# Performance work log

Measured on AMD Instinct MI355X. Metric: run time of the kernel, lower is better.

The kernel has to match this reference:

```python
import jax, jax.numpy as jnp
import numpy as np
import math

B, C, H, W = 8, 64, 256, 256
E, NH = 256, 8
HD = E // NH  # 32


def get_coords(h, w):
    xx, yy = jnp.meshgrid(jnp.arange(h, dtype=jnp.float32), jnp.arange(w, dtype=jnp.float32), indexing='ij')
    return jnp.stack((xx.reshape(-1), yy.reshape(-1)), axis=-1)  # [N, 2]


def setup_inputs() -> dict:
    key = jax.random.key(0)
    ks = jax.random.split(key, 12)
    def xavier(k, shape):
        fan_out, fan_in = shape
        a = math.sqrt(6.0 / (fan_in + fan_out))
        return jax.random.uniform(k, shape, jnp.float32, -a, a)
    x = jax.random.normal(ks[0], (B, C, H, W), jnp.float32)
    z = jax.random.normal(ks[1], (B, C), jnp.float32)
    pos = jax.random.uniform(ks[2], (B, NH, 2), jnp.float32) * (H - 1)
    Wq = xavier(ks[3], (E, C)); bq = jnp.zeros((E,), jnp.float32)
    Wk = xavier(ks[4], (E, C)); bk = jnp.zeros((E,), jnp.float32)
    Wv = xavier(ks[5], (E, C)); bv = jnp.zeros((E,), jnp.float32)
    Wp = xavier(ks[6], (HD, 2)); bp = jax.random.uniform(ks[7], (HD,), jnp.float32, -1.0, 1.0) / math.sqrt(2.0)
    return {"x": x, "z": z, "pos": pos, "Wq": Wq, "bq": bq, "Wk": Wk, "bk": bk,
            "Wv": Wv, "bv": bv, "Wp": Wp, "bp": bp}


def reference(x, z, pos, Wq, bq, Wk, bk, Wv, bv, Wp, bp):
    b, c, h, w = x.shape
    n = h * w
    x_flat = x.reshape(b, c, n).transpose(0, 2, 1)          # [B, N, C]
    pos_grid = get_coords(h, w)                              # [N, 2]
    q = (z @ Wq.T + bq).reshape(b, NH, HD)                   # [B, H, hd]
    k = (x_flat @ Wk.T + bk).reshape(b, n, NH, HD)           # [B, N, H, hd]
    # relative-position modulation of keys
    rel = pos_grid[None, :, None, :] - pos[:, None, :, :]    # [B, N, H, 2]
    qxk = rel @ Wp.T + bp                                    # [B, N, H, hd]
    k = k * qxk
    v = x_flat @ Wv.T + bv                                   # [B, N, E]
    attn_logits = jnp.einsum('bhc,bnhc->bnh', q, k) / math.sqrt(HD)
    attention = jax.nn.softmax(attn_logits, axis=1)          # softmax over N
    pos_out = jnp.einsum('bnh,nx->bhx', attention, pos_grid) # [B, H, 2]
    values = jnp.einsum('bnh,bnc->bhc', attention, v)        # [B, H, E]
    return (values, pos_out)
```

## Files before the change

kernel.cpp:

```cpp
#include <hip/hip_runtime.h>

#define NN    65536
#define NSUB  128
#define NBLK  (NN/NSUB)

typedef short bf16x8 __attribute__((ext_vector_type(8)));
typedef float f32x4v __attribute__((ext_vector_type(4)));
typedef unsigned short ushort_t;
typedef unsigned int uint_t;

#define XSTR   72
#define XHI_B  0
#define XLO_B  18432
#define LGA_B  18432
#define LGSTR  28
#define PSTR   136
#define RED_B  36864
#define SMEM_BYTES 37056

#define WTHI_B  0
#define WTLO_B  32768
#define CJ_B    65536
#define PM_B    66304
#define PL_B    197376
#define PSP_B   328448
#define PSX_B   590592
#define Q_B     8979200
#define QSTR    68

__device__ __forceinline__ uint_t bf16_rne_bits(float f) {
  uint_t u = __float_as_uint(f);
  return (u + 0x7FFFu + ((u >> 16) & 1u)) >> 16;
}
template <int CTRL>
__device__ __forceinline__ float dpp_add(float x) {
  int t = __builtin_amdgcn_update_dpp(0, __float_as_int(x), CTRL, 0xf, 0xf, false);
  return x + __int_as_float(t);
}
template <int CTRL>
__device__ __forceinline__ float dpp_maxs(float x) {
  int t = __builtin_amdgcn_update_dpp((int)0xFF800000u, __float_as_int(x), CTRL, 0xf, 0xf, false);
  return fmaxf(x, __int_as_float(t));
}
__device__ __forceinline__ float wave_sum(float x) {
  x = dpp_add<0x111>(x); x = dpp_add<0x112>(x); x = dpp_add<0x114>(x);
  x = dpp_add<0x118>(x); x = dpp_add<0x142>(x); x = dpp_add<0x143>(x);
  return __int_as_float(__builtin_amdgcn_readlane(__float_as_int(x), 63));
}
__device__ __forceinline__ float wave_max(float x) {
  x = dpp_maxs<0x111>(x); x = dpp_maxs<0x112>(x); x = dpp_maxs<0x114>(x);
  x = dpp_maxs<0x118>(x); x = dpp_maxs<0x142>(x); x = dpp_maxs<0x143>(x);
  return __int_as_float(__builtin_amdgcn_readlane(__float_as_int(x), 63));
}

__global__ __launch_bounds__(64) void prep_kernel(
    const float* __restrict__ z,  const float* __restrict__ Wq, const float* __restrict__ bq,
    const float* __restrict__ Wk, const float* __restrict__ bk,
    const float* __restrict__ Wp, const float* __restrict__ bp,
    ushort_t* __restrict__ WThi, ushort_t* __restrict__ WTlo, float* __restrict__ Cj)
{
  const int h = blockIdx.x, b = blockIdx.y, t = threadIdx.x;
  __shared__ float q[32];
  if (t < 32) {
    const int e = h*32 + t;
    float a = bq[e];
    const float* zr = z + b*64;
    const float* wr = Wq + e*64;
    #pragma unroll 8
    for (int c = 0; c < 64; ++c) a += zr[c]*wr[c];
    q[t] = a;
  }
  __syncthreads();
  const int c = t;
  float w[3] = {0.f, 0.f, 0.f};
  #pragma unroll 4
  for (int hd = 0; hd < 32; ++hd) {
    const float qk = q[hd] * Wk[(h*32+hd)*64 + c];
    w[0] += qk * bp[hd];
    w[1] += qk * Wp[hd*2+0];
    w[2] += qk * Wp[hd*2+1];
  }
  #pragma unroll
  for (int j = 0; j < 3; ++j) {
    const int coeff = h*3 + j;
    const uint_t hb = bf16_rne_bits(w[j]);
    const float  fh = __uint_as_float(hb << 16);
    const uint_t lb = bf16_rne_bits(w[j] - fh);
    WThi[(b*32 + coeff)*64 + c] = (ushort_t)hb;
    WTlo[(b*32 + coeff)*64 + c] = (ushort_t)lb;
  }
  if (h == 0) {
    #pragma unroll
    for (int r = 0; r < 8; ++r) {
      WThi[(b*32 + 24 + r)*64 + c] = 0;
      WTlo[(b*32 + 24 + r)*64 + c] = 0;
    }
  }
  if (t < 3) {
    float s = 0.f;
    for (int hd = 0; hd < 32; ++hd) {
      const float m = (t == 0) ? bp[hd] : Wp[hd*2 + (t-1)];
      s += q[hd] * m * bk[h*32+hd];
    }
    Cj[b*24 + h*3 + t] = s;
  }
}

__global__ __launch_bounds__(256, 4) void main_kernel(
    const float* __restrict__ x, const float* __restrict__ pos,
    const ushort_t* __restrict__ WThi, const ushort_t* __restrict__ WTlo,
    const float* __restrict__ Cj,
    float* __restrict__ Pm, float* __restrict__ Pl,
    float* __restrict__ Psp, float* __restrict__ Psx)
{
  extern __shared__ char smc[];
  ushort_t* xhi = (ushort_t*)(smc + XHI_B);
  float*    lga = (float*)(smc + LGA_B);
  float*    red = (float*)(smc + RED_B);
  const int t   = threadIdx.x;
  const int blk = blockIdx.x;
  const int b   = blockIdx.y;
  const int n0  = blk * NSUB;
  const int wid = t >> 6, lid = t & 63;
  const int c0  = lid & 15, q4 = lid >> 4;
  const int px  = t & 127;
  const int hgrp = t >> 7;
  const int half = wid & 1;

  bf16x8 bh[2][2], bl[2][2];
  {
    const ushort_t* wtb_h = WThi + b*2048;
    const ushort_t* wtb_l = WTlo + b*2048;
    #pragma unroll
    for (int nt = 0; nt < 2; ++nt)
      #pragma unroll
      for (int ks = 0; ks < 2; ++ks) {
        const int off = (nt*16 + c0)*64 + ks*32 + q4*8;
        bh[nt][ks] = *(const bf16x8*)(wtb_h + off);
        bl[nt][ks] = *(const bf16x8*)(wtb_l + off);
      }
  }

  {
    const float* xg = x + (size_t)b*64*NN + (size_t)hgrp*32*NN + n0 + px;
    float v[32];
    #pragma unroll
    for (int i = 0; i < 32; ++i) v[i] = xg[(size_t)i*NN];
    #pragma unroll
    for (int cc = 0; cc < 2; ++cc) {
      uint_t hb[16], lb[16];
      #pragma unroll
      for (int i = 0; i < 16; ++i) {
        const float f = v[cc*16+i];
        hb[i] = bf16_rne_bits(f);
        lb[i] = __float_as_uint(f - __uint_as_float(hb[i] << 16)) >> 16;
      }
      uint4 H0 = make_uint4(hb[0]|(hb[1]<<16), hb[2]|(hb[3]<<16), hb[4]|(hb[5]<<16), hb[6]|(hb[7]<<16));
      uint4 H1 = make_uint4(hb[8]|(hb[9]<<16), hb[10]|(hb[11]<<16), hb[12]|(hb[13]<<16), hb[14]|(hb[15]<<16));
      uint4 L0 = make_uint4(lb[0]|(lb[1]<<16), lb[2]|(lb[3]<<16), lb[4]|(lb[5]<<16), lb[6]|(lb[7]<<16));
      uint4 L1 = make_uint4(lb[8]|(lb[9]<<16), lb[10]|(lb[11]<<16), lb[12]|(lb[13]<<16), lb[14]|(lb[15]<<16));
      char* dh = smc + XHI_B + px*144 + (hgrp*2+cc)*32;
      char* dl = smc + XLO_B + px*144 + (hgrp*2+cc)*32;
      *(uint4*)(dh)      = H0;  *(uint4*)(dh + 16) = H1;
      *(uint4*)(dl)      = L0;  *(uint4*)(dl + 16) = L1;
    }
  }

  float cj[12];
  {
    const float* cjp = Cj + b*24 + hgrp*12;
    #pragma unroll
    for (int k = 0; k < 12; ++k) cj[k] = cjp[k];
  }
  const int gx = blk >> 1;
  float rxh[4], py[4];
  #pragma unroll
  for (int hl = 0; hl < 4; ++hl) {
    const int h = hgrp*4 + hl;
    rxh[hl] = (float)gx - pos[(b*8+h)*2 + 0];
    py[hl]  = pos[(b*8+h)*2 + 1];
  }

  __syncthreads();

  f32x4v acc[2][2];
  #pragma unroll
  for (int mt = 0; mt < 2; ++mt) { acc[mt][0] = (f32x4v)0.f; acc[mt][1] = (f32x4v)0.f; }
  {
    const int mrow0 = wid*32;
    #pragma unroll
    for (int mt = 0; mt < 2; ++mt) {
      const int row = mrow0 + mt*16 + c0;
      const ushort_t* ph = xhi + row*XSTR + q4*8;
      const ushort_t* pl = (ushort_t*)(smc + XLO_B) + row*XSTR + q4*8;
      bf16x8 ah0 = *(const bf16x8*)(ph);
      bf16x8 ah1 = *(const bf16x8*)(ph + 32);
      bf16x8 al0 = *(const bf16x8*)(pl);
      bf16x8 al1 = *(const bf16x8*)(pl + 32);
      #pragma unroll
      for (int nt = 0; nt < 2; ++nt) {
        f32x4v a = acc[mt][nt];
        a = __builtin_amdgcn_mfma_f32_16x16x32_bf16(ah0, bh[nt][0], a, 0, 0, 0);
        a = __builtin_amdgcn_mfma_f32_16x16x32_bf16(ah1, bh[nt][1], a, 0, 0, 0);
        a = __builtin_amdgcn_mfma_f32_16x16x32_bf16(ah0, bl[nt][0], a, 0, 0, 0);
        a = __builtin_amdgcn_mfma_f32_16x16x32_bf16(ah1, bl[nt][1], a, 0, 0, 0);
        a = __builtin_amdgcn_mfma_f32_16x16x32_bf16(al0, bh[nt][0], a, 0, 0, 0);
        a = __builtin_amdgcn_mfma_f32_16x16x32_bf16(al1, bh[nt][1], a, 0, 0, 0);
        acc[mt][nt] = a;
      }
    }
  }
  __syncthreads();

  {
    const int mrow0 = wid*32;
    #pragma unroll
    for (int mt = 0; mt < 2; ++mt)
      #pragma unroll
      for (int r = 0; r < 4; ++r) {
        const int prow = mrow0 + mt*16 + q4*4 + r;
        lga[prow*LGSTR + c0] = acc[mt][0][r];
        if (c0 < 8) lga[prow*LGSTR + 16 + c0] = acc[mt][1][r];
      }
  }
  __syncthreads();

  float a12[12];
  {
    const float4* ap = (const float4*)(lga + px*LGSTR + hgrp*12);
    #pragma unroll
    for (int r = 0; r < 3; ++r) *(float4*)(a12 + 4*r) = ap[r];
  }
  const float tf = (float)(((blk & 1) << 7) + px);
  float lg[4];
  #pragma unroll
  for (int hl = 0; hl < 4; ++hl) {
    const float a0 = a12[hl*3+0] + cj[hl*3+0];
    const float a1 = a12[hl*3+1] + cj[hl*3+1];
    const float a2 = a12[hl*3+2] + cj[hl*3+2];
    lg[hl] = (a0 + rxh[hl]*a1 + (tf - py[hl])*a2) * 0.17677669529663687f;
  }

  #pragma unroll
  for (int hl = 0; hl < 4; ++hl) {
    const float m = wave_max(lg[hl]);
    if (lid == 0) red[(hgrp*4 + hl)*2 + half] = m;
  }
  __syncthreads();

  float p[4];
  #pragma unroll
  for (int hl = 0; hl < 4; ++hl) {
    const int h = hgrp*4 + hl;
    const float M = fmaxf(red[h*2+0], red[h*2+1]);
    p[hl] = __expf(lg[hl] - M);
  }

  {
    ushort_t* pls = (ushort_t*)(smc + LGA_B);
    #pragma unroll
    for (int hl = 0; hl < 4; ++hl) {
      const int h = hgrp*4 + hl;
      const uint_t hb = bf16_rne_bits(p[hl]);
      const float  hf = __uint_as_float(hb << 16);
      const uint_t lb = __float_as_uint(p[hl] - hf) >> 16;
      pls[h*PSTR + px]       = (ushort_t)hb;
      pls[(h+8)*PSTR + px]   = (ushort_t)lb;
    }
  }

  #pragma unroll
  for (int hl = 0; hl < 4; ++hl) {
    const int h = hgrp*4 + hl;
    const float sp  = wave_sum(p[hl]);
    const float spj = wave_sum(p[hl] * tf);
    if (lid == 0) { red[16 + h*2 + half] = sp; red[32 + h*2 + half] = spj; }
  }
  __syncthreads();

  if (t < 8) {
    const int base = (b*NBLK + blk)*8 + t;
    const float M  = fmaxf(red[t*2+0], red[t*2+1]);
    const float L  = red[16+t*2+0] + red[16+t*2+1];
    const float SJ = red[32+t*2+0] + red[32+t*2+1];
    Pm[base] = M;
    Pl[base] = L;
    Psp[base*2+0] = (float)gx * L;
    Psp[base*2+1] = SJ;
  }

  {
    const ushort_t* pls = (const ushort_t*)(smc + LGA_B);
    bf16x8 afr[4];
    #pragma unroll
    for (int ks = 0; ks < 4; ++ks)
      afr[ks] = *(const bf16x8*)(pls + c0*PSTR + ks*32 + q4*8);

    f32x4v accB = (f32x4v)0.f;
    const int chbase = wid*16 + c0;
    #pragma unroll
    for (int ks = 0; ks < 4; ++ks) {
      const ushort_t* xcol = xhi + (ks*32 + q4*8)*XSTR + chbase;
      bf16x8 bfr;
      #pragma unroll
      for (int i = 0; i < 8; ++i) bfr[i] = (short)xcol[i*XSTR];
      accB = __builtin_amdgcn_mfma_f32_16x16x32_bf16(afr[ks], bfr, accB, 0, 0, 0);
    }

    const size_t pb64 = ((size_t)(b*NBLK + blk))*8*64;
    #pragma unroll
    for (int r = 0; r < 4; ++r) {
      const float o = __shfl_xor(accB[r], 32, 64);
      if (q4 < 2) {
        const int h = q4*4 + r;
        Psx[pb64 + h*64 + chbase] = accB[r] + o;
      }
    }
  }
}

__global__ __launch_bounds__(256) void reduce1_kernel(
    const float* __restrict__ Pm, const float* __restrict__ Pl,
    const float* __restrict__ Psp, const float* __restrict__ Psx,
    float* __restrict__ Q)
{
  const int g = blockIdx.x, h = blockIdx.y, b = blockIdx.z, t = threadIdx.x;
  __shared__ float al[64];
  __shared__ float mgs;
  __shared__ float sums[3];
  __shared__ float sxl[256];
  const int base = (b*NBLK + g*64)*8 + h;

  float m_t = -1e30f;
  if (t < 64) {
    m_t = Pm[base + t*8];
    float mm = m_t;
    #pragma unroll
    for (int off = 32; off >= 1; off >>= 1) mm = fmaxf(mm, __shfl_xor(mm, off, 64));
    if (t == 0) mgs = mm;
  }
  __syncthreads();
  const float Mg = mgs;
  if (t < 64) {
    const float a = __expf(m_t - Mg);
    al[t] = a;
    float lt = Pl[base + t*8] * a;
    float sx = Psp[(base + t*8)*2 + 0] * a;
    float sy = Psp[(base + t*8)*2 + 1] * a;
    #pragma unroll
    for (int off = 32; off >= 1; off >>= 1) {
      lt += __shfl_xor(lt, off, 64);
      sx += __shfl_xor(sx, off, 64);
      sy += __shfl_xor(sy, off, 64);
    }
    if (t == 0) { sums[0] = lt; sums[1] = sx; sums[2] = sy; }
  }
  __syncthreads();
  {
    const int c = t & 63, g2 = t >> 6;
    float acc = 0.f;
    #pragma unroll
    for (int i = 0; i < 16; ++i) {
      const int k = g2*16 + i;
      acc += al[k] * Psx[(size_t)(base + k*8)*64 + c];
    }
    sxl[g2*64 + c] = acc;
  }
  __syncthreads();
  float* q = Q + ((b*8 + h)*8 + g)*QSTR;
  if (t < 64) q[4+t] = sxl[t] + sxl[64+t] + sxl[128+t] + sxl[192+t];
  if (t == 0) { q[0] = Mg; q[1] = sums[0]; q[2] = sums[1]; q[3] = sums[2]; }
}

__global__ __launch_bounds__(64) void reduce2_kernel(
    const float* __restrict__ Q, const float* __restrict__ Wv, const float* __restrict__ bv,
    float* __restrict__ out)
{
  const int h = blockIdx.x, b = blockIdx.y, t = threadIdx.x;
  __shared__ float qm[8], bl[8], l8[8], sx8[8], sy8[8];
  __shared__ float SXs[64];
  const float* qb = Q + ((b*8 + h)*8)*QSTR;

  if (t < 8) qm[t] = qb[t*QSTR + 0];
  __syncthreads();
  float M = qm[0];
  #pragma unroll
  for (int g = 1; g < 8; ++g) M = fmaxf(M, qm[g]);
  if (t < 8) {
    const float be = __expf(qm[t] - M);
    bl[t]  = be;
    l8[t]  = be * qb[t*QSTR + 1];
    sx8[t] = be * qb[t*QSTR + 2];
    sy8[t] = be * qb[t*QSTR + 3];
  }
  __syncthreads();
  float L = 0.f;
  #pragma unroll
  for (int g = 0; g < 8; ++g) L += l8[g];
  const float invL = 1.0f / L;
  {
    float s = 0.f;
    #pragma unroll
    for (int g = 0; g < 8; ++g) s += bl[g] * qb[g*QSTR + 4 + t];
    SXs[t] = s * invL;
  }
  __syncthreads();

  #pragma unroll
  for (int r = 0; r < 4; ++r) {
    const int e = t + 64*r;
    float v = bv[e];
    const float* wvr = Wv + e*64;
    #pragma unroll 8
    for (int c = 0; c < 64; ++c) v += wvr[c] * SXs[c];
    out[(b*8 + h)*256 + e] = v;
  }
  if (t == 0) {
    float spx = 0.f, spy = 0.f;
    #pragma unroll
    for (int g = 0; g < 8; ++g) { spx += sx8[g]; spy += sy8[g]; }
    out[16384 + (b*8 + h)*2 + 0] = spx * invL;
    out[16384 + (b*8 + h)*2 + 1] = spy * invL;
  }
}

extern "C" void kernel_launch(void* const* d_in, const int* in_sizes, int n_in,
                              void* d_out, int out_size, void* d_ws, size_t ws_size,
                              hipStream_t stream)
{
  const float* x   = (const float*)d_in[0];
  const float* z   = (const float*)d_in[1];
  const float* pos = (const float*)d_in[2];
  const float* Wq  = (const float*)d_in[3];
  const float* bq  = (const float*)d_in[4];
  const float* Wk  = (const float*)d_in[5];
  const float* bk  = (const float*)d_in[6];
  const float* Wv  = (const float*)d_in[7];
  const float* bv  = (const float*)d_in[8];
  const float* Wp  = (const float*)d_in[9];
  const float* bp  = (const float*)d_in[10];
  float* out = (float*)d_out;
  char*  wsb = (char*)d_ws;

  ushort_t* WThi = (ushort_t*)(wsb + WTHI_B);
  ushort_t* WTlo = (ushort_t*)(wsb + WTLO_B);
  float* Cj  = (float*)(wsb + CJ_B);
  float* Pm  = (float*)(wsb + PM_B);
  float* Pl  = (float*)(wsb + PL_B);
  float* Psp = (float*)(wsb + PSP_B);
  float* Psx = (float*)(wsb + PSX_B);
  float* Q   = (float*)(wsb + Q_B);

  prep_kernel   <<<dim3(8,8),    64,  0,          stream>>>(z, Wq, bq, Wk, bk, Wp, bp, WThi, WTlo, Cj);
  main_kernel   <<<dim3(NBLK,8), 256, SMEM_BYTES, stream>>>(x, pos, WThi, WTlo, Cj, Pm, Pl, Psp, Psx);
  reduce1_kernel<<<dim3(8,8,8),  256, 0,          stream>>>(Pm, Pl, Psp, Psx, Q);
  reduce2_kernel<<<dim3(8,8),    64,  0,          stream>>>(Q, Wv, bv, out);
}
```

Baseline: 234.6 us.

## Vectorize x loads, use packed bf16 convert, and swizzle LDS layout

The x tile is now read with 16-byte vector loads, each thread taking 4 consecutive pixels across 8 channels, where before each thread did scalar per-pixel loads over 32 channels. The hi bf16 split uses the hardware v_cvt_pk_bf16_f32 instruction, and the lo residual is packed with a byte permute. LDS stores use an XOR swizzle on 16-byte chunks, and the MFMA A-fragment reads and column reads index through the same swizzle to avoid bank conflicts. This should cut global load instruction count and LDS bank conflicts. The price is more complex addressing, which must stay consistent between writer and readers.

```diff
diff --git a/kernel.cpp b/kernel.cpp
--- a/kernel.cpp
+++ b/kernel.cpp
@@ -31,6 +31,11 @@
 __device__ __forceinline__ uint_t bf16_rne_bits(float f) {
   uint_t u = __float_as_uint(f);
   return (u + 0x7FFFu + ((u >> 16) & 1u)) >> 16;
+}
+__device__ __forceinline__ uint_t cvt_pk_bf16(float a, float b) {
+  uint_t r;
+  asm("v_cvt_pk_bf16_f32 %0, %1, %2" : "=v"(r) : "v"(a), "v"(b));
+  return r;
 }
 template <int CTRL>
 __device__ __forceinline__ float dpp_add(float x) {
@@ -114,7 +119,6 @@
     float* __restrict__ Psp, float* __restrict__ Psx)
 {
   extern __shared__ char smc[];
-  ushort_t* xhi = (ushort_t*)(smc + XHI_B);
   float*    lga = (float*)(smc + LGA_B);
   float*    red = (float*)(smc + RED_B);
   const int t   = threadIdx.x;
@@ -142,27 +146,32 @@
   }
 
   {
-    const float* xg = x + (size_t)b*64*NN + (size_t)hgrp*32*NN + n0 + px;
-    float v[32];
-    #pragma unroll
-    for (int i = 0; i < 32; ++i) v[i] = xg[(size_t)i*NN];
-    #pragma unroll
-    for (int cc = 0; cc < 2; ++cc) {
-      uint_t hb[16], lb[16];
+    const int qd  = t & 31;
+    const int g   = t >> 5;
+    const int swz = (qd >> 1) & 7;
+    const int chnk = (g ^ swz) * 16;
+    const float* xg = x + (size_t)b*64*NN + (size_t)g*8*NN + n0 + 4*qd;
+    f32x4v v[8];
+    #pragma unroll
+    for (int j = 0; j < 8; ++j) v[j] = *(const f32x4v*)(xg + (size_t)j*NN);
+    #pragma unroll
+    for (int i = 0; i < 4; ++i) {
+      uint_t H[4], L[4];
       #pragma unroll
-      for (int i = 0; i < 16; ++i) {
-        const float f = v[cc*16+i];
-        hb[i] = bf16_rne_bits(f);
-        lb[i] = __float_as_uint(f - __uint_as_float(hb[i] << 16)) >> 16;
+      for (int jp = 0; jp < 4; ++jp) {
+        const float f0 = v[2*jp][i], f1 = v[2*jp+1][i];
+        const uint_t hpk = cvt_pk_bf16(f0, f1);
+        const float h0 = __uint_as_float(hpk << 16);
+        const float h1 = __uint_as_float(hpk & 0xFFFF0000u);
+        const uint_t l0 = __float_as_uint(f0 - h0);
+        const uint_t l1 = __float_as_uint(f1 - h1);
+        H[jp] = hpk;
+        L[jp] = __builtin_amdgcn_perm(l1, l0, 0x07060302u);
       }
-      uint4 H0 = make_uint4(hb[0]|(hb[1]<<16), hb[2]|(hb[3]<<16), hb[4]|(hb[5]<<16), hb[6]|(hb[7]<<16));
-      uint4 H1 = make_uint4(hb[8]|(hb[9]<<16), hb[10]|(hb[11]<<16), hb[12]|(hb[13]<<16), hb[14]|(hb[15]<<16));
-      uint4 L0 = make_uint4(lb[0]|(lb[1]<<16), lb[2]|(lb[3]<<16), lb[4]|(lb[5]<<16), lb[6]|(lb[7]<<16));
-      uint4 L1 = make_uint4(lb[8]|(lb[9]<<16), lb[10]|(lb[11]<<16), lb[12]|(lb[13]<<16), lb[14]|(lb[15]<<16));
-      char* dh = smc + XHI_B + px*144 + (hgrp*2+cc)*32;
-      char* dl = smc + XLO_B + px*144 + (hgrp*2+cc)*32;
-      *(uint4*)(dh)      = H0;  *(uint4*)(dh + 16) = H1;
-      *(uint4*)(dl)      = L0;  *(uint4*)(dl + 16) = L1;
+      char* dh = smc + XHI_B + (4*qd + i)*144 + chnk;
+      char* dl = smc + XLO_B + (4*qd + i)*144 + chnk;
+      *(uint4*)dh = make_uint4(H[0], H[1], H[2], H[3]);
+      *(uint4*)dl = make_uint4(L[0], L[1], L[2], L[3]);
     }
   }
 
@@ -190,13 +199,15 @@
     const int mrow0 = wid*32;
     #pragma unroll
     for (int mt = 0; mt < 2; ++mt) {
-      const int row = mrow0 + mt*16 + c0;
-      const ushort_t* ph = xhi + row*XSTR + q4*8;
-      const ushort_t* pl = (ushort_t*)(smc + XLO_B) + row*XSTR + q4*8;
-      bf16x8 ah0 = *(const bf16x8*)(ph);
-      bf16x8 ah1 = *(const bf16x8*)(ph + 32);
-      bf16x8 al0 = *(const bf16x8*)(pl);
-      bf16x8 al1 = *(const bf16x8*)(pl + 32);
+      const int row  = mrow0 + mt*16 + c0;
+      const int srow = (4*wid + 2*mt + (c0 >> 3)) & 7;
+      const int ch0  = (q4 ^ srow) * 16;
+      const char* rh = smc + XHI_B + row*144;
+      const char* rl = smc + XLO_B + row*144;
+      bf16x8 ah0 = *(const bf16x8*)(rh + ch0);
+      bf16x8 ah1 = *(const bf16x8*)(rh + (ch0 ^ 64));
+      bf16x8 al0 = *(const bf16x8*)(rl + ch0);
+      bf16x8 al1 = *(const bf16x8*)(rl + (ch0 ^ 64));
       #pragma unroll
       for (int nt = 0; nt < 2; ++nt) {
         f32x4v a = acc[mt][nt];
@@ -298,12 +309,13 @@
 
     f32x4v accB = (f32x4v)0.f;
     const int chbase = wid*16 + c0;
+    const int cbase = (((2*wid + (c0 >> 3)) ^ q4) * 16) + (c0 & 7) * 2;
     #pragma unroll
     for (int ks = 0; ks < 4; ++ks) {
-      const ushort_t* xcol = xhi + (ks*32 + q4*8)*XSTR + chbase;
+      const char* xc = smc + XHI_B + (ks*32 + q4*8)*144 + (cbase ^ ((ks & 1) * 64));
       bf16x8 bfr;
       #pragma unroll
-      for (int i = 0; i < 8; ++i) bfr[i] = (short)xcol[i*XSTR];
+      for (int i = 0; i < 8; ++i) bfr[i] = *(const short*)(xc + i*144);
       accB = __builtin_amdgcn_mfma_f32_16x16x32_bf16(afr[ks], bfr, accB, 0, 0, 0);
     }
 
```

Result: no change. 234.8 us (+0.1%).

## Stream x tile through LDS via async global_load_lds double buffering

Applied to the files above, without the earlier changes.

Replaces the per-thread strided loads of 32 channels into registers with direct global-to-LDS async loads in four 16-channel chunks. Two fp32 staging buffers let the split into bf16 hi/lo of one chunk overlap the load of the next. The split now uses the packed v_cvt_pk_bf16_f32 instruction and a byte permute instead of manual rounding. LDS use grows by 16 KB and the occupancy hint drops from 4 to 3 blocks per CU. The extra barriers also add sync overhead.

```diff
diff --git a/kernel.cpp b/kernel.cpp
--- a/kernel.cpp
+++ b/kernel.cpp
@@ -15,8 +15,9 @@
 #define LGA_B  18432
 #define LGSTR  28
 #define PSTR   136
-#define RED_B  36864
-#define SMEM_BYTES 37056
+#define F32C_B 36864
+#define RED_B  53248
+#define SMEM_BYTES 53632
 
 #define WTHI_B  0
 #define WTLO_B  32768
@@ -31,6 +32,11 @@
 __device__ __forceinline__ uint_t bf16_rne_bits(float f) {
   uint_t u = __float_as_uint(f);
   return (u + 0x7FFFu + ((u >> 16) & 1u)) >> 16;
+}
+__device__ __forceinline__ uint_t cvt_pk_bf16(float a, float b) {
+  uint_t r;
+  asm("v_cvt_pk_bf16_f32 %0, %1, %2" : "=v"(r) : "v"(a), "v"(b));
+  return r;
 }
 template <int CTRL>
 __device__ __forceinline__ float dpp_add(float x) {
@@ -106,7 +112,45 @@
   }
 }
 
-__global__ __launch_bounds__(256, 4) void main_kernel(
+#define ISSUE_CHUNK(CI)                                                              \
+  do {                                                                               \
+    _Pragma("unroll")                                                                \
+    for (int k = 0; k < 2; ++k) {                                                    \
+      const int p  = wid*2 + k;                                                      \
+      const int ch = (CI)*16 + 2*p + (lid >> 5);                                     \
+      const float* gsrc = xbb + (size_t)ch*NN + (lid & 31)*4;                        \
+      char* ldst = smc + F32C_B + ((CI)&1)*8192 + p*1024;                            \
+      __builtin_amdgcn_global_load_lds(                                              \
+          (const __attribute__((address_space(1))) void*)gsrc,                       \
+          (__attribute__((address_space(3))) void*)ldst, 16, 0, 0);                  \
+    }                                                                                \
+  } while (0)
+
+#define CONVERT_CHUNK(CI)                                                            \
+  do {                                                                               \
+    const float* f32c = (const float*)(smc + F32C_B + ((CI)&1)*8192);                \
+    float vv[8];                                                                     \
+    _Pragma("unroll")                                                                \
+    for (int j = 0; j < 8; ++j) vv[j] = f32c[(hgrp*8 + j)*128 + px];                 \
+    uint_t H[4], L[4];                                                               \
+    _Pragma("unroll")                                                                \
+    for (int jp = 0; jp < 4; ++jp) {                                                 \
+      const float f0 = vv[2*jp], f1 = vv[2*jp+1];                                    \
+      const uint_t hpk = cvt_pk_bf16(f0, f1);                                        \
+      const float h0 = __uint_as_float(hpk << 16);                                   \
+      const float h1 = __uint_as_float(hpk & 0xFFFF0000u);                           \
+      const uint_t l0 = __float_as_uint(f0 - h0);                                    \
+      const uint_t l1 = __float_as_uint(f1 - h1);                                    \
+      H[jp] = hpk;                                                                   \
+      L[jp] = __builtin_amdgcn_perm(l1, l0, 0x07060302u);                            \
+    }                                                                                \
+    char* dh = smc + XHI_B + px*144 + ((CI)*2 + hgrp)*16;                            \
+    char* dl = smc + XLO_B + px*144 + ((CI)*2 + hgrp)*16;                            \
+    *(uint4*)dh = make_uint4(H[0], H[1], H[2], H[3]);                                \
+    *(uint4*)dl = make_uint4(L[0], L[1], L[2], L[3]);                                \
+  } while (0)
+
+__global__ __launch_bounds__(256, 3) void main_kernel(
     const float* __restrict__ x, const float* __restrict__ pos,
     const ushort_t* __restrict__ WThi, const ushort_t* __restrict__ WTlo,
     const float* __restrict__ Cj,
@@ -114,7 +158,6 @@
     float* __restrict__ Psp, float* __restrict__ Psx)
 {
   extern __shared__ char smc[];
-  ushort_t* xhi = (ushort_t*)(smc + XHI_B);
   float*    lga = (float*)(smc + LGA_B);
   float*    red = (float*)(smc + RED_B);
   const int t   = threadIdx.x;
@@ -140,32 +183,6 @@
         bl[nt][ks] = *(const bf16x8*)(wtb_l + off);
       }
   }
-
-  {
-    const float* xg = x + (size_t)b*64*NN + (size_t)hgrp*32*NN + n0 + px;
-    float v[32];
-    #pragma unroll
-    for (int i = 0; i < 32; ++i) v[i] = xg[(size_t)i*NN];
-    #pragma unroll
-    for (int cc = 0; cc < 2; ++cc) {
-      uint_t hb[16], lb[16];
-      #pragma unroll
-      for (int i = 0; i < 16; ++i) {
-        const float f = v[cc*16+i];
-        hb[i] = bf16_rne_bits(f);
-        lb[i] = __float_as_uint(f - __uint_as_float(hb[i] << 16)) >> 16;
-      }
-      uint4 H0 = make_uint4(hb[0]|(hb[1]<<16), hb[2]|(hb[3]<<16), hb[4]|(hb[5]<<16), hb[6]|(hb[7]<<16));
-      uint4 H1 = make_uint4(hb[8]|(hb[9]<<16), hb[10]|(hb[11]<<16), hb[12]|(hb[13]<<16), hb[14]|(hb[15]<<16));
-      uint4 L0 = make_uint4(lb[0]|(lb[1]<<16), lb[2]|(lb[3]<<16), lb[4]|(lb[5]<<16), lb[6]|(lb[7]<<16));
-      uint4 L1 = make_uint4(lb[8]|(lb[9]<<16), lb[10]|(lb[11]<<16), lb[12]|(lb[13]<<16), lb[14]|(lb[15]<<16));
-      char* dh = smc + XHI_B + px*144 + (hgrp*2+cc)*32;
-      char* dl = smc + XLO_B + px*144 + (hgrp*2+cc)*32;
-      *(uint4*)(dh)      = H0;  *(uint4*)(dh + 16) = H1;
-      *(uint4*)(dl)      = L0;  *(uint4*)(dl + 16) = L1;
-    }
-  }
-
   float cj[12];
   {
     const float* cjp = Cj + b*24 + hgrp*12;
@@ -181,7 +198,38 @@
     py[hl]  = pos[(b*8+h)*2 + 1];
   }
 
-  __syncthreads();
+  const float* xbb = x + (size_t)b*64*NN + n0;
+  ISSUE_CHUNK(0);
+  ISSUE_CHUNK(1);
+
+  asm volatile("s_waitcnt vmcnt(2)" ::: "memory");
+  __builtin_amdgcn_sched_barrier(0);
+  __builtin_amdgcn_s_barrier();
+  CONVERT_CHUNK(0);
+  asm volatile("s_waitcnt lgkmcnt(0)" ::: "memory");
+  __builtin_amdgcn_s_barrier();
+  ISSUE_CHUNK(2);
+
+  asm volatile("s_waitcnt vmcnt(2)" ::: "memory");
+  __builtin_amdgcn_sched_barrier(0);
+  __builtin_amdgcn_s_barrier();
+  CONVERT_CHUNK(1);
+  asm volatile("s_waitcnt lgkmcnt(0)" ::: "memory");
+  __builtin_amdgcn_s_barrier();
+  ISSUE_CHUNK(3);
+
+  asm volatile("s_waitcnt vmcnt(2)" ::: "memory");
+  __builtin_amdgcn_sched_barrier(0);
+  __builtin_amdgcn_s_barrier();
+  CONVERT_CHUNK(2);
+
+  asm volatile("s_waitcnt vmcnt(0)" ::: "memory");
+  __builtin_amdgcn_sched_barrier(0);
+  __builtin_amdgcn_s_barrier();
+  CONVERT_CHUNK(3);
+
+  asm volatile("s_waitcnt lgkmcnt(0)" ::: "memory");
+  __builtin_amdgcn_s_barrier();
 
   f32x4v acc[2][2];
   #pragma unroll
@@ -191,8 +239,8 @@
     #pragma unroll
     for (int mt = 0; mt < 2; ++mt) {
       const int row = mrow0 + mt*16 + c0;
-      const ushort_t* ph = xhi + row*XSTR + q4*8;
-      const ushort_t* pl = (ushort_t*)(smc + XLO_B) + row*XSTR + q4*8;
+      const ushort_t* ph = (const ushort_t*)(smc + XHI_B) + row*XSTR + q4*8;
+      const ushort_t* pl = (const ushort_t*)(smc + XLO_B) + row*XSTR + q4*8;
       bf16x8 ah0 = *(const bf16x8*)(ph);
       bf16x8 ah1 = *(const bf16x8*)(ph + 32);
       bf16x8 al0 = *(const bf16x8*)(pl);
@@ -300,7 +348,7 @@
     const int chbase = wid*16 + c0;
     #pragma unroll
     for (int ks = 0; ks < 4; ++ks) {
-      const ushort_t* xcol = xhi + (ks*32 + q4*8)*XSTR + chbase;
+      const ushort_t* xcol = (const ushort_t*)(smc + XHI_B) + (ks*32 + q4*8)*XSTR + chbase;
       bf16x8 bfr;
       #pragma unroll
       for (int i = 0; i < 8; ++i) bfr[i] = (short)xcol[i*XSTR];
```

Result: no change. 233.2 us (median of 2 runs) (-0.6%).
